# Performance work log

Measured on AMD Instinct MI355X. Metric: run time of the kernel, lower is better.

## Reference

```python
import math
import jax, jax.numpy as jnp
import numpy as np

BH, S, DK = 64, 1024, 64   # batch*heads, seq_len, head dim
FG, FL = 32, 32            # global / local enrichment feature dims
H, B = 16, 4               # mask layout [heads, batch, seq]


def setup_inputs() -> dict:
    key = jax.random.key(0)
    k1, k2, k3, k4, k5, k6 = jax.random.split(key, 6)
    return {
        "query": jax.random.normal(k1, (BH, S, DK), dtype=jnp.float32),
        "key": jax.random.normal(k2, (BH, S, DK), dtype=jnp.float32),
        "value": jax.random.normal(k3, (BH, S, DK), dtype=jnp.float32),
        "local_f": jax.random.normal(k4, (BH, S, FL), dtype=jnp.float32),
        "global_f": jax.random.normal(k5, (BH, S, FG), dtype=jnp.float32),
        "mask": jax.random.randint(k6, (H, B, S), 0, 2, dtype=jnp.int32),
    }


def reference(query, key, value, local_f, global_f, mask):
    dk = query.shape[-1]
    # enrich q/k with global then local features (matches torch concat order)
    pq = jnp.concatenate([query, global_f, local_f], axis=2)   # [BH, S, dk+fg+fl]
    pk = jnp.concatenate([key, global_f, local_f], axis=2)
    scores = jnp.einsum("bqd,bkd->bqk", pq, pk) / math.sqrt(dk)  # [BH, S, S]
    # mask [H, B, S] -> [H*B, S] -> broadcast over query positions
    m = mask.reshape(-1, mask.shape[-1])[:, None, :]            # [H*B, 1, S]
    scores = jnp.where(m == 1, jnp.float32(-1e9), scores)
    attn = jax.nn.softmax(scores, axis=-1)
    return jnp.einsum("bqk,bkd->bqd", attn, value)              # [BH, S, dk]
```

## Files before the change

kernel.cpp:

```cpp
#include <hip/hip_runtime.h>
#include <hip/hip_bf16.h>


#define BHn 64
#define Sn  1024
#define NT  16
#define KSTR 152
#define VSTR 72
#define KTILE (64*KSTR*2)
#define VTILE (64*VSTR*2)
#define BUFSZ (KTILE+VTILE)
#define OSTR 68
#define WAIT_VM0 0x0F70

typedef __attribute__((ext_vector_type(8)))  __bf16 bf16x8;
typedef __attribute__((ext_vector_type(16))) float  f32x16;
typedef __attribute__((ext_vector_type(4)))  unsigned int u32x4;

__device__ __forceinline__ unsigned f2bf1(float a){
    union { float f; unsigned u; } c; c.f = a;
    return (c.u + 0x7fffu + ((c.u >> 16) & 1u)) >> 16;
}
__device__ __forceinline__ unsigned f2bf2(float a, float b){
    return f2bf1(a) | (f2bf1(b) << 16);
}
__device__ __forceinline__ unsigned pkbf(float a, float b){
    return __builtin_amdgcn_perm(__builtin_bit_cast(unsigned, b),
                                 __builtin_bit_cast(unsigned, a), 0x07060302u);
}
__device__ __forceinline__ void gld_lds16(const void* g, void* l){
    __builtin_amdgcn_global_load_lds(
        (const __attribute__((address_space(1))) unsigned int*)g,
        (__attribute__((address_space(3))) unsigned int*)l, 16, 0, 0);
}

__global__ __launch_bounds__(256)
void attn_prep(const float* __restrict__ K, const float* __restrict__ V,
               const float* __restrict__ LF, const float* __restrict__ GF,
               const int* __restrict__ M,
               unsigned short* __restrict__ Kp, unsigned short* __restrict__ Vp)
{
    __shared__ __align__(16) unsigned char plds[BUFSZ];
    unsigned short* kl = (unsigned short*)plds;
    unsigned int*   vl = (unsigned int*)(plds + KTILE);

    const int tid = threadIdx.x;
    const int bh = blockIdx.x >> 4, ti = blockIdx.x & 15, kb = ti*64;

    #pragma unroll
    for (int i=0;i<2;i++){
        int idx = tid + 256*i, row = idx>>3, c = idx&7;
        const float* s = K + ((size_t)bh*Sn + kb + row)*64 + c*8;
        float4 f0 = *(const float4*)s, f1 = *(const float4*)(s+4);
        u32x4 w; w[0]=f2bf2(f0.x,f0.y); w[1]=f2bf2(f0.z,f0.w);
        w[2]=f2bf2(f1.x,f1.y); w[3]=f2bf2(f1.z,f1.w);
        *(u32x4*)(kl + row*KSTR + c*8) = w;
    }
    {
        int row = tid>>2, c = tid&3;
        const float* s = GF + ((size_t)bh*Sn + kb + row)*32 + c*8;
        float4 f0 = *(const float4*)s, f1 = *(const float4*)(s+4);
        u32x4 w; w[0]=f2bf2(f0.x,f0.y); w[1]=f2bf2(f0.z,f0.w);
        w[2]=f2bf2(f1.x,f1.y); w[3]=f2bf2(f1.z,f1.w);
        *(u32x4*)(kl + row*KSTR + 64 + c*8) = w;
    }
    {
        int row = tid>>2, c = tid&3;
        const float* s = LF + ((size_t)bh*Sn + kb + row)*32 + c*8;
        float4 f0 = *(const float4*)s, f1 = *(const float4*)(s+4);
        u32x4 w; w[0]=f2bf2(f0.x,f0.y); w[1]=f2bf2(f0.z,f0.w);
        w[2]=f2bf2(f1.x,f1.y); w[3]=f2bf2(f1.z,f1.w);
        *(u32x4*)(kl + row*KSTR + 96 + c*8) = w;
    }
    if (tid < 64){
        int mv = M[(size_t)bh*Sn + kb + tid];
        u32x4 w; w[0] = (mv == 1) ? 0x0000ceacu : 0u;
        w[1]=0u; w[2]=0u; w[3]=0u;
        *(u32x4*)(kl + tid*KSTR + 128) = w;
        u32x4 z; z[0]=0u; z[1]=0u; z[2]=0u; z[3]=0u;
        *(u32x4*)(kl + tid*KSTR + 136) = z;
        *(u32x4*)(kl + tid*KSTR + 144) = z;
    }
    {
        int d = tid & 63, g = tid >> 6;
        const float* vb = V + ((size_t)bh*Sn + kb + 16*g)*64 + d;
        const int pm[16] = {0,1,2,3, 8,9,10,11, 4,5,6,7, 12,13,14,15};
        unsigned w[8];
        #pragma unroll
        for (int m=0;m<8;m++)
            w[m] = f2bf2(vb[(size_t)pm[2*m]*64], vb[(size_t)pm[2*m+1]*64]);
        u32x4 a, b;
        a[0]=w[0]; a[1]=w[1]; a[2]=w[2]; a[3]=w[3];
        b[0]=w[4]; b[1]=w[5]; b[2]=w[6]; b[3]=w[7];
        *(u32x4*)(vl + d*36 + g*8)     = a;
        *(u32x4*)(vl + d*36 + g*8 + 4) = b;
        u32x4 z; z[0]=0u; z[1]=0u; z[2]=0u; z[3]=0u;
        *(u32x4*)(vl + d*36 + 32) = z;
    }
    __syncthreads();

    unsigned char* dK = (unsigned char*)Kp + (size_t)(bh*NT + ti)*KTILE;
    unsigned char* dV = (unsigned char*)Vp + (size_t)(bh*NT + ti)*VTILE;
    #pragma unroll
    for (int i=0;i<4;i++){
        int off = tid*16 + i*4096;
        *(u32x4*)(dK + off) = *(const u32x4*)(plds + off);
    }
    {
        int off = tid*16 + 4*4096;
        if (off < KTILE) *(u32x4*)(dK + off) = *(const u32x4*)(plds + off);
    }
    #pragma unroll
    for (int i=0;i<2;i++){
        int off = tid*16 + i*4096;
        *(u32x4*)(dV + off) = *(const u32x4*)(plds + KTILE + off);
    }
    {
        int off = tid*16 + 2*4096;
        if (off < VTILE) *(u32x4*)(dV + off) = *(const u32x4*)(plds + KTILE + off);
    }
}

__global__ __launch_bounds__(512, 4)
void attn_main(const float* __restrict__ Q, const unsigned short* __restrict__ Kp,
               const unsigned short* __restrict__ Vp,
               const float* __restrict__ GF, const float* __restrict__ LF,
               float* __restrict__ O)
{
    __shared__ __align__(16) unsigned char smem[2*BUFSZ];
    const int tid  = threadIdx.x;
    const int wave = tid >> 6, lane = tid & 63;
    const int l31  = lane & 31, h = lane >> 5;
    const int qh   = wave >> 1;
    const int kp   = wave & 1;
    const int bh = blockIdx.x & 63;
    const int qb = blockIdx.x >> 6;
    const float SCL = 0.18033688011112042f;

    const int qrow = qb*128 + qh*32 + l31;
    u32x4 qf[9];
    #pragma unroll
    for (int dc = 0; dc < 8; dc++){
        const int cb = dc*16 + 8*h;
        const float* src;
        if (cb < 64)      src = Q  + ((size_t)bh*Sn + qrow)*64 + cb;
        else if (cb < 96) src = GF + ((size_t)bh*Sn + qrow)*32 + (cb - 64);
        else              src = LF + ((size_t)bh*Sn + qrow)*32 + (cb - 96);
        float4 f0 = *(const float4*)src;
        float4 f1 = *(const float4*)(src + 4);
        qf[dc][0] = f2bf2(f0.x*SCL, f0.y*SCL);
        qf[dc][1] = f2bf2(f0.z*SCL, f0.w*SCL);
        qf[dc][2] = f2bf2(f1.x*SCL, f1.y*SCL);
        qf[dc][3] = f2bf2(f1.z*SCL, f1.w*SCL);
    }
    qf[8][0] = h ? 0u : 0x00003f80u;
    qf[8][1] = 0u; qf[8][2] = 0u; qf[8][3] = 0u;

    f32x16 oacc[2];
    #pragma unroll
    for (int dt=0; dt<2; dt++)
        #pragma unroll
        for (int r=0; r<16; r++) oacc[dt][r] = 0.f;
    float lrun = 0.f;

    const unsigned char* gKb = (const unsigned char*)Kp + (size_t)bh*NT*KTILE;
    const unsigned char* gVb = (const unsigned char*)Vp + (size_t)bh*NT*VTILE;

    #pragma unroll
    for (int i=0;i<4;i++){
        int c = wave + 8*i;
        if (c < 19)      gld_lds16(gKb + (size_t)c*1024 + lane*16, smem + c*1024);
        else if (c < 28) gld_lds16(gVb + (size_t)(c-19)*1024 + lane*16,
                                   smem + KTILE + (size_t)(c-19)*1024);
    }
    __builtin_amdgcn_s_waitcnt(WAIT_VM0);

    for (int t = 0; t < NT; t++){
        unsigned char* cur = smem + (size_t)(t&1)*BUFSZ;
        unsigned char* nxt = smem + (size_t)((t+1)&1)*BUFSZ;
        __syncthreads();
        if (t+1 < NT){
            const unsigned char* gK = gKb + (size_t)(t+1)*KTILE;
            const unsigned char* gV = gVb + (size_t)(t+1)*VTILE;
            #pragma unroll
            for (int i=0;i<4;i++){
                int c = wave + 8*i;
                if (c < 19)      gld_lds16(gK + (size_t)c*1024 + lane*16, nxt + c*1024);
                else if (c < 28) gld_lds16(gV + (size_t)(c-19)*1024 + lane*16,
                                           nxt + KTILE + (size_t)(c-19)*1024);
            }
        }
        unsigned short* kt_s = (unsigned short*)cur;
        unsigned short* vt_s = (unsigned short*)(cur + KTILE);

        f32x16 acc;
        #pragma unroll
        for (int r=0;r<16;r++) acc[r] = 0.f;
        #pragma unroll
        for (int dc=0; dc<9; dc++){
            u32x4 ar = *(const u32x4*)(kt_s + (kp*32 + l31)*KSTR + dc*16 + 8*h);
            acc = __builtin_amdgcn_mfma_f32_32x32x16_bf16(
                    __builtin_bit_cast(bf16x8, ar),
                    __builtin_bit_cast(bf16x8, qf[dc]), acc, 0, 0, 0);
        }

        float rs = 0.f;
        #pragma unroll
        for (int r=0;r<16;r++){
            float p = __builtin_amdgcn_exp2f(acc[r]);
            acc[r] = p; rs += p;
        }
        lrun += rs;

        unsigned pk[8];
        #pragma unroll
        for (int i=0;i<8;i++) pk[i] = pkbf(acc[2*i], acc[2*i+1]);
        u32x4 b0, b1;
        b0[0]=pk[0]; b0[1]=pk[1]; b0[2]=pk[2]; b0[3]=pk[3];
        b1[0]=pk[4]; b1[1]=pk[5]; b1[2]=pk[6]; b1[3]=pk[7];

        #pragma unroll
        for (int dt=0;dt<2;dt++){
            u32x4 va0 = *(const u32x4*)(vt_s + (dt*32 + l31)*VSTR + kp*32 + 8*h);
            u32x4 va1 = *(const u32x4*)(vt_s + (dt*32 + l31)*VSTR + kp*32 + 16 + 8*h);
            oacc[dt] = __builtin_amdgcn_mfma_f32_32x32x16_bf16(
                    __builtin_bit_cast(bf16x8, va0),
                    __builtin_bit_cast(bf16x8, b0), oacc[dt], 0, 0, 0);
            oacc[dt] = __builtin_amdgcn_mfma_f32_32x32x16_bf16(
                    __builtin_bit_cast(bf16x8, va1),
                    __builtin_bit_cast(bf16x8, b1), oacc[dt], 0, 0, 0);
        }

        __builtin_amdgcn_s_waitcnt(WAIT_VM0);
    }

    __syncthreads();
    float lw = lrun + __shfl_xor(lrun, 32, 64);
    float* s1 = (float*)smem;
    float* s2 = (float*)(smem + 128*OSTR*4);
    if (kp == 1){
        #pragma unroll
        for (int dt=0;dt<2;dt++)
            #pragma unroll
            for (int rg=0;rg<4;rg++){
                float4 w;
                w.x = oacc[dt][rg*4+0]; w.y = oacc[dt][rg*4+1];
                w.z = oacc[dt][rg*4+2]; w.w = oacc[dt][rg*4+3];
                *(float4*)(s1 + (qh*32 + l31)*OSTR + dt*32 + rg*8 + 4*h) = w;
            }
        if (h == 0) s2[qh*32 + l31] = lw;
    }
    __syncthreads();
    if (kp == 0){
        float inv = 1.0f / (lw + s2[qh*32 + l31]);
        #pragma unroll
        for (int dt=0;dt<2;dt++)
            #pragma unroll
            for (int rg=0;rg<4;rg++){
                float* p = s1 + (qh*32 + l31)*OSTR + dt*32 + rg*8 + 4*h;
                float4 w = *(float4*)p;
                w.x = (w.x + oacc[dt][rg*4+0])*inv;
                w.y = (w.y + oacc[dt][rg*4+1])*inv;
                w.z = (w.z + oacc[dt][rg*4+2])*inv;
                w.w = (w.w + oacc[dt][rg*4+3])*inv;
                *(float4*)p = w;
            }
    }
    __syncthreads();
    #pragma unroll
    for (int i=0;i<4;i++){
        int idx = tid + 512*i, r = idx>>4, c = idx&15;
        *(float4*)(O + ((size_t)bh*Sn + qb*128 + r)*64 + c*4) =
            *(const float4*)(s1 + r*OSTR + c*4);
    }
}

extern "C" void kernel_launch(void* const* d_in, const int* in_sizes, int n_in,
                              void* d_out, int out_size, void* d_ws, size_t ws_size,
                              hipStream_t stream) {
    const float* Q  = (const float*)d_in[0];
    const float* K  = (const float*)d_in[1];
    const float* V  = (const float*)d_in[2];
    const float* LF = (const float*)d_in[3];
    const float* GF = (const float*)d_in[4];
    const int*   M  = (const int*)d_in[5];
    float* O = (float*)d_out;

    unsigned short* Kp = (unsigned short*)d_ws;
    unsigned short* Vp = Kp + (size_t)BHn*NT*64*KSTR;

    attn_prep<<<dim3(BHn*NT), dim3(256), 0, stream>>>(K, V, LF, GF, M, Kp, Vp);
    attn_main<<<dim3(BHn*(Sn/128)), dim3(512), 0, stream>>>(Q, Kp, Vp, GF, LF, O);
}
```

Before: 140.7 us.

## Halve block to 4 waves, each computing two 32-row query subtiles

The main attention kernel now launches 256 threads (4 waves) per block instead of 512. Each wave handles two 32-row query subtiles and reuses every K and V fragment it reads from shared memory for two MFMAs, which halves LDS read traffic per FLOP. Each wave now issues 7 global-to-LDS loads per tile instead of up to 4, and the MFMA phases are wrapped in s_setprio. The cost is roughly double the accumulator and Q-fragment registers per wave and half as many waves per block to hide latency.

After: 144.3 us. 1.03x slower.

```diff
diff --git a/kernel.cpp b/kernel.cpp
--- a/kernel.cpp
+++ b/kernel.cpp
@@ -121,7 +121,7 @@
     }
 }
 
-__global__ __launch_bounds__(512, 4)
+__global__ __launch_bounds__(256, 2)
 void attn_main(const float* __restrict__ Q, const unsigned short* __restrict__ Kp,
                const unsigned short* __restrict__ Vp,
                const float* __restrict__ GF, const float* __restrict__ LF,
@@ -131,47 +131,53 @@
     const int tid  = threadIdx.x;
     const int wave = tid >> 6, lane = tid & 63;
     const int l31  = lane & 31, h = lane >> 5;
-    const int qh   = wave >> 1;
+    const int qp   = wave >> 1;
     const int kp   = wave & 1;
     const int bh = blockIdx.x & 63;
     const int qb = blockIdx.x >> 6;
     const float SCL = 0.18033688011112042f;
 
-    const int qrow = qb*128 + qh*32 + l31;
-    u32x4 qf[9];
-    #pragma unroll
-    for (int dc = 0; dc < 8; dc++){
-        const int cb = dc*16 + 8*h;
-        const float* src;
-        if (cb < 64)      src = Q  + ((size_t)bh*Sn + qrow)*64 + cb;
-        else if (cb < 96) src = GF + ((size_t)bh*Sn + qrow)*32 + (cb - 64);
-        else              src = LF + ((size_t)bh*Sn + qrow)*32 + (cb - 96);
-        float4 f0 = *(const float4*)src;
-        float4 f1 = *(const float4*)(src + 4);
-        qf[dc][0] = f2bf2(f0.x*SCL, f0.y*SCL);
-        qf[dc][1] = f2bf2(f0.z*SCL, f0.w*SCL);
-        qf[dc][2] = f2bf2(f1.x*SCL, f1.y*SCL);
-        qf[dc][3] = f2bf2(f1.z*SCL, f1.w*SCL);
-    }
-    qf[8][0] = h ? 0u : 0x00003f80u;
-    qf[8][1] = 0u; qf[8][2] = 0u; qf[8][3] = 0u;
-
-    f32x16 oacc[2];
-    #pragma unroll
-    for (int dt=0; dt<2; dt++)
-        #pragma unroll
-        for (int r=0; r<16; r++) oacc[dt][r] = 0.f;
-    float lrun = 0.f;
+    u32x4 qf[2][8];
+    #pragma unroll
+    for (int sub = 0; sub < 2; sub++){
+        const int qrow = qb*128 + qp*64 + sub*32 + l31;
+        #pragma unroll
+        for (int dc = 0; dc < 8; dc++){
+            const int cb = dc*16 + 8*h;
+            const float* src;
+            if (cb < 64)      src = Q  + ((size_t)bh*Sn + qrow)*64 + cb;
+            else if (cb < 96) src = GF + ((size_t)bh*Sn + qrow)*32 + (cb - 64);
+            else              src = LF + ((size_t)bh*Sn + qrow)*32 + (cb - 96);
+            float4 f0 = *(const float4*)src;
+            float4 f1 = *(const float4*)(src + 4);
+            qf[sub][dc][0] = f2bf2(f0.x*SCL, f0.y*SCL);
+            qf[sub][dc][1] = f2bf2(f0.z*SCL, f0.w*SCL);
+            qf[sub][dc][2] = f2bf2(f1.x*SCL, f1.y*SCL);
+            qf[sub][dc][3] = f2bf2(f1.z*SCL, f1.w*SCL);
+        }
+    }
+    u32x4 qfb;
+    qfb[0] = h ? 0u : 0x00003f80u;
+    qfb[1] = 0u; qfb[2] = 0u; qfb[3] = 0u;
+
+    f32x16 oacc[2][2];
+    #pragma unroll
+    for (int sub=0; sub<2; sub++)
+        #pragma unroll
+        for (int dt=0; dt<2; dt++)
+            #pragma unroll
+            for (int r=0; r<16; r++) oacc[sub][dt][r] = 0.f;
+    float lrun0 = 0.f, lrun1 = 0.f;
 
     const unsigned char* gKb = (const unsigned char*)Kp + (size_t)bh*NT*KTILE;
     const unsigned char* gVb = (const unsigned char*)Vp + (size_t)bh*NT*VTILE;
 
     #pragma unroll
-    for (int i=0;i<4;i++){
-        int c = wave + 8*i;
-        if (c < 19)      gld_lds16(gKb + (size_t)c*1024 + lane*16, smem + c*1024);
-        else if (c < 28) gld_lds16(gVb + (size_t)(c-19)*1024 + lane*16,
-                                   smem + KTILE + (size_t)(c-19)*1024);
+    for (int i=0;i<7;i++){
+        int c = wave + 4*i;
+        if (c < 19) gld_lds16(gKb + (size_t)c*1024 + lane*16, smem + c*1024);
+        else        gld_lds16(gVb + (size_t)(c-19)*1024 + lane*16,
+                              smem + KTILE + (size_t)(c-19)*1024);
     }
     __builtin_amdgcn_s_waitcnt(WAIT_VM0);
 
@@ -183,93 +189,133 @@
             const unsigned char* gK = gKb + (size_t)(t+1)*KTILE;
             const unsigned char* gV = gVb + (size_t)(t+1)*VTILE;
             #pragma unroll
-            for (int i=0;i<4;i++){
-                int c = wave + 8*i;
-                if (c < 19)      gld_lds16(gK + (size_t)c*1024 + lane*16, nxt + c*1024);
-                else if (c < 28) gld_lds16(gV + (size_t)(c-19)*1024 + lane*16,
-                                           nxt + KTILE + (size_t)(c-19)*1024);
+            for (int i=0;i<7;i++){
+                int c = wave + 4*i;
+                if (c < 19) gld_lds16(gK + (size_t)c*1024 + lane*16, nxt + c*1024);
+                else        gld_lds16(gV + (size_t)(c-19)*1024 + lane*16,
+                                      nxt + KTILE + (size_t)(c-19)*1024);
             }
         }
         unsigned short* kt_s = (unsigned short*)cur;
         unsigned short* vt_s = (unsigned short*)(cur + KTILE);
 
-        f32x16 acc;
-        #pragma unroll
-        for (int r=0;r<16;r++) acc[r] = 0.f;
-        #pragma unroll
-        for (int dc=0; dc<9; dc++){
+        f32x16 acc0, acc1;
+        #pragma unroll
+        for (int r=0;r<16;r++){ acc0[r] = 0.f; acc1[r] = 0.f; }
+        __builtin_amdgcn_s_setprio(1);
+        #pragma unroll
+        for (int dc=0; dc<8; dc++){
             u32x4 ar = *(const u32x4*)(kt_s + (kp*32 + l31)*KSTR + dc*16 + 8*h);
-            acc = __builtin_amdgcn_mfma_f32_32x32x16_bf16(
+            acc0 = __builtin_amdgcn_mfma_f32_32x32x16_bf16(
                     __builtin_bit_cast(bf16x8, ar),
-                    __builtin_bit_cast(bf16x8, qf[dc]), acc, 0, 0, 0);
-        }
-
-        float rs = 0.f;
+                    __builtin_bit_cast(bf16x8, qf[0][dc]), acc0, 0, 0, 0);
+            acc1 = __builtin_amdgcn_mfma_f32_32x32x16_bf16(
+                    __builtin_bit_cast(bf16x8, ar),
+                    __builtin_bit_cast(bf16x8, qf[1][dc]), acc1, 0, 0, 0);
+        }
+        {
+            u32x4 ab = *(const u32x4*)(kt_s + (kp*32 + l31)*KSTR + 128 + 8*h);
+            acc0 = __builtin_amdgcn_mfma_f32_32x32x16_bf16(
+                    __builtin_bit_cast(bf16x8, ab),
+                    __builtin_bit_cast(bf16x8, qfb), acc0, 0, 0, 0);
+            acc1 = __builtin_amdgcn_mfma_f32_32x32x16_bf16(
+                    __builtin_bit_cast(bf16x8, ab),
+                    __builtin_bit_cast(bf16x8, qfb), acc1, 0, 0, 0);
+        }
+        __builtin_amdgcn_s_setprio(0);
+
+        float rs0 = 0.f, rs1 = 0.f;
         #pragma unroll
         for (int r=0;r<16;r++){
-            float p = __builtin_amdgcn_exp2f(acc[r]);
-            acc[r] = p; rs += p;
-        }
-        lrun += rs;
-
-        unsigned pk[8];
-        #pragma unroll
-        for (int i=0;i<8;i++) pk[i] = pkbf(acc[2*i], acc[2*i+1]);
-        u32x4 b0, b1;
-        b0[0]=pk[0]; b0[1]=pk[1]; b0[2]=pk[2]; b0[3]=pk[3];
-        b1[0]=pk[4]; b1[1]=pk[5]; b1[2]=pk[6]; b1[3]=pk[7];
-
+            float p0 = __builtin_amdgcn_exp2f(acc0[r]);
+            float p1 = __builtin_amdgcn_exp2f(acc1[r]);
+            acc0[r] = p0; rs0 += p0;
+            acc1[r] = p1; rs1 += p1;
+        }
+        lrun0 += rs0; lrun1 += rs1;
+
+        unsigned pk0[8], pk1[8];
+        #pragma unroll
+        for (int i=0;i<8;i++){
+            pk0[i] = pkbf(acc0[2*i], acc0[2*i+1]);
+            pk1[i] = pkbf(acc1[2*i], acc1[2*i+1]);
+        }
+        u32x4 b00, b01, b10, b11;
+        b00[0]=pk0[0]; b00[1]=pk0[1]; b00[2]=pk0[2]; b00[3]=pk0[3];
+        b01[0]=pk0[4]; b01[1]=pk0[5]; b01[2]=pk0[6]; b01[3]=pk0[7];
+        b10[0]=pk1[0]; b10[1]=pk1[1]; b10[2]=pk1[2]; b10[3]=pk1[3];
+        b11[0]=pk1[4]; b11[1]=pk1[5]; b11[2]=pk1[6]; b11[3]=pk1[7];
+
+        __builtin_amdgcn_s_setprio(1);
         #pragma unroll
         for (int dt=0;dt<2;dt++){
             u32x4 va0 = *(const u32x4*)(vt_s + (dt*32 + l31)*VSTR + kp*32 + 8*h);
             u32x4 va1 = *(const u32x4*)(vt_s + (dt*32 + l31)*VSTR + kp*32 + 16 + 8*h);
-            oacc[dt] = __builtin_amdgcn_mfma_f32_32x32x16_bf16(
+            oacc[0][dt] = __builtin_amdgcn_mfma_f32_32x32x16_bf16(
                     __builtin_bit_cast(bf16x8, va0),
-                    __builtin_bit_cast(bf16x8, b0), oacc[dt], 0, 0, 0);
-            oacc[dt] = __builtin_amdgcn_mfma_f32_32x32x16_bf16(
+                    __builtin_bit_cast(bf16x8, b00), oacc[0][dt], 0, 0, 0);
+            oacc[0][dt] = __builtin_amdgcn_mfma_f32_32x32x16_bf16(
                     __builtin_bit_cast(bf16x8, va1),
-                    __builtin_bit_cast(bf16x8, b1), oacc[dt], 0, 0, 0);
-        }
+                    __builtin_bit_cast(bf16x8, b01), oacc[0][dt], 0, 0, 0);
+            oacc[1][dt] = __builtin_amdgcn_mfma_f32_32x32x16_bf16(
+                    __builtin_bit_cast(bf16x8, va0),
+                    __builtin_bit_cast(bf16x8, b10), oacc[1][dt], 0, 0, 0);
+            oacc[1][dt] = __builtin_amdgcn_mfma_f32_32x32x16_bf16(
+                    __builtin_bit_cast(bf16x8, va1),
+                    __builtin_bit_cast(bf16x8, b11), oacc[1][dt], 0, 0, 0);
+        }
+        __builtin_amdgcn_s_setprio(0);
 
         __builtin_amdgcn_s_waitcnt(WAIT_VM0);
     }
 
     __syncthreads();
-    float lw = lrun + __shfl_xor(lrun, 32, 64);
+    float lw0 = lrun0 + __shfl_xor(lrun0, 32, 64);
+    float lw1 = lrun1 + __shfl_xor(lrun1, 32, 64);
     float* s1 = (float*)smem;
     float* s2 = (float*)(smem + 128*OSTR*4);
     if (kp == 1){
         #pragma unroll
-        for (int dt=0;dt<2;dt++)
+        for (int sub=0;sub<2;sub++)
             #pragma unroll
-            for (int rg=0;rg<4;rg++){
-                float4 w;
-                w.x = oacc[dt][rg*4+0]; w.y = oacc[dt][rg*4+1];
-                w.z = oacc[dt][rg*4+2]; w.w = oacc[dt][rg*4+3];
-                *(float4*)(s1 + (qh*32 + l31)*OSTR + dt*32 + rg*8 + 4*h) = w;
-            }
-        if (h == 0) s2[qh*32 + l31] = lw;
+            for (int dt=0;dt<2;dt++)
+                #pragma unroll
+                for (int rg=0;rg<4;rg++){
+                    float4 w;
+                    w.x = oacc[sub][dt][rg*4+0]; w.y = oacc[sub][dt][rg*4+1];
+                    w.z = oacc[sub][dt][rg*4+2]; w.w = oacc[sub][dt][rg*4+3];
+                    *(float4*)(s1 + (qp*64 + sub*32 + l31)*OSTR + dt*32 + rg*8 + 4*h) = w;
+                }
+        if (h == 0){
+            s2[qp*64 + l31]      = lw0;
+            s2[qp*64 + 32 + l31] = lw1;
+        }
     }
     __syncthreads();
     if (kp == 0){
-        float inv = 1.0f / (lw + s2[qh*32 + l31]);
-        #pragma unroll
-        for (int dt=0;dt<2;dt++)
+        float inv0 = 1.0f / (lw0 + s2[qp*64 + l31]);
+        float inv1 = 1.0f / (lw1 + s2[qp*64 + 32 + l31]);
+        #pragma unroll
+        for (int sub=0;sub<2;sub++){
+            float inv = sub ? inv1 : inv0;
             #pragma unroll
-            for (int rg=0;rg<4;rg++){
-                float* p = s1 + (qh*32 + l31)*OSTR + dt*32 + rg*8 + 4*h;
-                float4 w = *(float4*)p;
-                w.x = (w.x + oacc[dt][rg*4+0])*inv;
-                w.y = (w.y + oacc[dt][rg*4+1])*inv;
-                w.z = (w.z + oacc[dt][rg*4+2])*inv;
-                w.w = (w.w + oacc[dt][rg*4+3])*inv;
-                *(float4*)p = w;
-            }
+            for (int dt=0;dt<2;dt++)
+                #pragma unroll
+                for (int rg=0;rg<4;rg++){
+                    float* p = s1 + (qp*64 + sub*32 + l31)*OSTR + dt*32 + rg*8 + 4*h;
+                    float4 w = *(float4*)p;
+                    w.x = (w.x + oacc[sub][dt][rg*4+0])*inv;
+                    w.y = (w.y + oacc[sub][dt][rg*4+1])*inv;
+                    w.z = (w.z + oacc[sub][dt][rg*4+2])*inv;
+                    w.w = (w.w + oacc[sub][dt][rg*4+3])*inv;
+                    *(float4*)p = w;
+                }
+        }
     }
     __syncthreads();
     #pragma unroll
-    for (int i=0;i<4;i++){
-        int idx = tid + 512*i, r = idx>>4, c = idx&15;
+    for (int i=0;i<8;i++){
+        int idx = tid + 256*i, r = idx>>4, c = idx&15;
         *(float4*)(O + ((size_t)bh*Sn + qb*128 + r)*64 + c*4) =
             *(const float4*)(s1 + r*OSTR + c*4);
     }
@@ -290,5 +336,5 @@
     unsigned short* Vp = Kp + (size_t)BHn*NT*64*KSTR;
 
     attn_prep<<<dim3(BHn*NT), dim3(256), 0, stream>>>(K, V, LF, GF, M, Kp, Vp);
-    attn_main<<<dim3(BHn*(Sn/128)), dim3(512), 0, stream>>>(Q, Kp, Vp, GF, LF, O);
-}
+    attn_main<<<dim3(BHn*(Sn/128)), dim3(256), 0, stream>>>(Q, Kp, Vp, GF, LF, O);
+}
```

## Pre-swizzle K/V tiles into MFMA fragment layout and load directly from global

Applied to the files above, without the earlier changes.

The prep kernel now writes K (with features and mask column) and V into a single packed buffer laid out exactly as the MFMA operand fragments each lane needs. The main kernel then reads operands straight from global/L2 with coalesced 16-byte loads instead of staging double-buffered tiles through LDS. This removes the per-tile barriers and LDS traffic and shrinks shared memory use. It also adds s_setprio around the MFMA bursts and a tree-reduced row sum. The risk is that global-load latency is no longer hidden by an explicit prefetch, and each K/V tile is now read by every wave separately through cache.

Measured after the change: 146.5 us. 4.1% more time.

```diff
diff --git a/kernel.cpp b/kernel.cpp
--- a/kernel.cpp
+++ b/kernel.cpp
@@ -5,13 +5,9 @@
 #define BHn 64
 #define Sn  1024
 #define NT  16
-#define KSTR 152
-#define VSTR 72
-#define KTILE (64*KSTR*2)
-#define VTILE (64*VSTR*2)
-#define BUFSZ (KTILE+VTILE)
+#define TILESZ 26624
+#define KIMG   18432
 #define OSTR 68
-#define WAIT_VM0 0x0F70
 
 typedef __attribute__((ext_vector_type(8)))  __bf16 bf16x8;
 typedef __attribute__((ext_vector_type(16))) float  f32x16;
@@ -28,21 +24,13 @@
     return __builtin_amdgcn_perm(__builtin_bit_cast(unsigned, b),
                                  __builtin_bit_cast(unsigned, a), 0x07060302u);
 }
-__device__ __forceinline__ void gld_lds16(const void* g, void* l){
-    __builtin_amdgcn_global_load_lds(
-        (const __attribute__((address_space(1))) unsigned int*)g,
-        (__attribute__((address_space(3))) unsigned int*)l, 16, 0, 0);
-}
 
 __global__ __launch_bounds__(256)
 void attn_prep(const float* __restrict__ K, const float* __restrict__ V,
                const float* __restrict__ LF, const float* __restrict__ GF,
-               const int* __restrict__ M,
-               unsigned short* __restrict__ Kp, unsigned short* __restrict__ Vp)
+               const int* __restrict__ M, unsigned short* __restrict__ P)
 {
-    __shared__ __align__(16) unsigned char plds[BUFSZ];
-    unsigned short* kl = (unsigned short*)plds;
-    unsigned int*   vl = (unsigned int*)(plds + KTILE);
+    __shared__ __align__(16) unsigned char plds[TILESZ];
 
     const int tid = threadIdx.x;
     const int bh = blockIdx.x >> 4, ti = blockIdx.x & 15, kb = ti*64;
@@ -54,32 +42,35 @@
         float4 f0 = *(const float4*)s, f1 = *(const float4*)(s+4);
         u32x4 w; w[0]=f2bf2(f0.x,f0.y); w[1]=f2bf2(f0.z,f0.w);
         w[2]=f2bf2(f1.x,f1.y); w[3]=f2bf2(f1.z,f1.w);
-        *(u32x4*)(kl + row*KSTR + c*8) = w;
-    }
-    {
-        int row = tid>>2, c = tid&3;
-        const float* s = GF + ((size_t)bh*Sn + kb + row)*32 + c*8;
+        int kp = row>>5, l31 = row&31, dc = c>>1, h = c&1;
+        *(u32x4*)(plds + ((kp*9+dc)*2+h)*512 + l31*16) = w;
+    }
+    {
+        int row = tid>>2, c2 = tid&3;
+        const float* s = GF + ((size_t)bh*Sn + kb + row)*32 + c2*8;
         float4 f0 = *(const float4*)s, f1 = *(const float4*)(s+4);
         u32x4 w; w[0]=f2bf2(f0.x,f0.y); w[1]=f2bf2(f0.z,f0.w);
         w[2]=f2bf2(f1.x,f1.y); w[3]=f2bf2(f1.z,f1.w);
-        *(u32x4*)(kl + row*KSTR + 64 + c*8) = w;
-    }
-    {
-        int row = tid>>2, c = tid&3;
-        const float* s = LF + ((size_t)bh*Sn + kb + row)*32 + c*8;
+        int kp = row>>5, l31 = row&31, dc = 4+(c2>>1), h = c2&1;
+        *(u32x4*)(plds + ((kp*9+dc)*2+h)*512 + l31*16) = w;
+    }
+    {
+        int row = tid>>2, c2 = tid&3;
+        const float* s = LF + ((size_t)bh*Sn + kb + row)*32 + c2*8;
         float4 f0 = *(const float4*)s, f1 = *(const float4*)(s+4);
         u32x4 w; w[0]=f2bf2(f0.x,f0.y); w[1]=f2bf2(f0.z,f0.w);
         w[2]=f2bf2(f1.x,f1.y); w[3]=f2bf2(f1.z,f1.w);
-        *(u32x4*)(kl + row*KSTR + 96 + c*8) = w;
+        int kp = row>>5, l31 = row&31, dc = 6+(c2>>1), h = c2&1;
+        *(u32x4*)(plds + ((kp*9+dc)*2+h)*512 + l31*16) = w;
     }
     if (tid < 64){
         int mv = M[(size_t)bh*Sn + kb + tid];
+        int kp = tid>>5, l31 = tid&31;
         u32x4 w; w[0] = (mv == 1) ? 0x0000ceacu : 0u;
         w[1]=0u; w[2]=0u; w[3]=0u;
-        *(u32x4*)(kl + tid*KSTR + 128) = w;
+        *(u32x4*)(plds + ((kp*9+8)*2+0)*512 + l31*16) = w;
         u32x4 z; z[0]=0u; z[1]=0u; z[2]=0u; z[3]=0u;
-        *(u32x4*)(kl + tid*KSTR + 136) = z;
-        *(u32x4*)(kl + tid*KSTR + 144) = z;
+        *(u32x4*)(plds + ((kp*9+8)*2+1)*512 + l31*16) = z;
     }
     {
         int d = tid & 63, g = tid >> 6;
@@ -92,42 +83,31 @@
         u32x4 a, b;
         a[0]=w[0]; a[1]=w[1]; a[2]=w[2]; a[3]=w[3];
         b[0]=w[4]; b[1]=w[5]; b[2]=w[6]; b[3]=w[7];
-        *(u32x4*)(vl + d*36 + g*8)     = a;
-        *(u32x4*)(vl + d*36 + g*8 + 4) = b;
-        u32x4 z; z[0]=0u; z[1]=0u; z[2]=0u; z[3]=0u;
-        *(u32x4*)(vl + d*36 + 32) = z;
-    }
-    __syncthreads();
-
-    unsigned char* dK = (unsigned char*)Kp + (size_t)(bh*NT + ti)*KTILE;
-    unsigned char* dV = (unsigned char*)Vp + (size_t)(bh*NT + ti)*VTILE;
-    #pragma unroll
-    for (int i=0;i<4;i++){
+        int kp = g>>1, j = g&1, dt = d>>5, l31 = d&31;
+        unsigned char* vs = plds + KIMG + (((kp*2+dt)*2+j)*2)*512 + l31*16;
+        *(u32x4*)(vs)       = a;
+        *(u32x4*)(vs + 512) = b;
+    }
+    __syncthreads();
+
+    unsigned char* dP = (unsigned char*)P + (size_t)(bh*NT + ti)*TILESZ;
+    #pragma unroll
+    for (int i=0;i<6;i++){
         int off = tid*16 + i*4096;
-        *(u32x4*)(dK + off) = *(const u32x4*)(plds + off);
-    }
-    {
-        int off = tid*16 + 4*4096;
-        if (off < KTILE) *(u32x4*)(dK + off) = *(const u32x4*)(plds + off);
-    }
-    #pragma unroll
-    for (int i=0;i<2;i++){
-        int off = tid*16 + i*4096;
-        *(u32x4*)(dV + off) = *(const u32x4*)(plds + KTILE + off);
-    }
-    {
-        int off = tid*16 + 2*4096;
-        if (off < VTILE) *(u32x4*)(dV + off) = *(const u32x4*)(plds + KTILE + off);
+        *(u32x4*)(dP + off) = *(const u32x4*)(plds + off);
+    }
+    {
+        int off = tid*16 + 6*4096;
+        if (off < TILESZ) *(u32x4*)(dP + off) = *(const u32x4*)(plds + off);
     }
 }
 
 __global__ __launch_bounds__(512, 4)
-void attn_main(const float* __restrict__ Q, const unsigned short* __restrict__ Kp,
-               const unsigned short* __restrict__ Vp,
+void attn_main(const float* __restrict__ Q, const unsigned short* __restrict__ P,
                const float* __restrict__ GF, const float* __restrict__ LF,
                float* __restrict__ O)
 {
-    __shared__ __align__(16) unsigned char smem[2*BUFSZ];
+    __shared__ __align__(16) unsigned char smem[128*OSTR*4 + 512];
     const int tid  = threadIdx.x;
     const int wave = tid >> 6, lane = tid & 63;
     const int l31  = lane & 31, h = lane >> 5;
@@ -163,75 +143,64 @@
         for (int r=0; r<16; r++) oacc[dt][r] = 0.f;
     float lrun = 0.f;
 
-    const unsigned char* gKb = (const unsigned char*)Kp + (size_t)bh*NT*KTILE;
-    const unsigned char* gVb = (const unsigned char*)Vp + (size_t)bh*NT*VTILE;
-
-    #pragma unroll
-    for (int i=0;i<4;i++){
-        int c = wave + 8*i;
-        if (c < 19)      gld_lds16(gKb + (size_t)c*1024 + lane*16, smem + c*1024);
-        else if (c < 28) gld_lds16(gVb + (size_t)(c-19)*1024 + lane*16,
-                                   smem + KTILE + (size_t)(c-19)*1024);
-    }
-    __builtin_amdgcn_s_waitcnt(WAIT_VM0);
+    const unsigned char* kptr = (const unsigned char*)P
+        + (size_t)bh*NT*TILESZ + kp*9216 + lane*16;
+    const unsigned char* vptr = (const unsigned char*)P
+        + (size_t)bh*NT*TILESZ + KIMG + kp*4096 + lane*16;
 
     for (int t = 0; t < NT; t++){
-        unsigned char* cur = smem + (size_t)(t&1)*BUFSZ;
-        unsigned char* nxt = smem + (size_t)((t+1)&1)*BUFSZ;
-        __syncthreads();
-        if (t+1 < NT){
-            const unsigned char* gK = gKb + (size_t)(t+1)*KTILE;
-            const unsigned char* gV = gVb + (size_t)(t+1)*VTILE;
-            #pragma unroll
-            for (int i=0;i<4;i++){
-                int c = wave + 8*i;
-                if (c < 19)      gld_lds16(gK + (size_t)c*1024 + lane*16, nxt + c*1024);
-                else if (c < 28) gld_lds16(gV + (size_t)(c-19)*1024 + lane*16,
-                                           nxt + KTILE + (size_t)(c-19)*1024);
-            }
-        }
-        unsigned short* kt_s = (unsigned short*)cur;
-        unsigned short* vt_s = (unsigned short*)(cur + KTILE);
+        const unsigned char* kt = kptr + (size_t)t*TILESZ;
+        const unsigned char* vt = vptr + (size_t)t*TILESZ;
 
         f32x16 acc;
         #pragma unroll
         for (int r=0;r<16;r++) acc[r] = 0.f;
+        __builtin_amdgcn_s_setprio(1);
         #pragma unroll
         for (int dc=0; dc<9; dc++){
-            u32x4 ar = *(const u32x4*)(kt_s + (kp*32 + l31)*KSTR + dc*16 + 8*h);
+            u32x4 ar = *(const u32x4*)(kt + dc*1024);
             acc = __builtin_amdgcn_mfma_f32_32x32x16_bf16(
                     __builtin_bit_cast(bf16x8, ar),
                     __builtin_bit_cast(bf16x8, qf[dc]), acc, 0, 0, 0);
         }
-
-        float rs = 0.f;
-        #pragma unroll
-        for (int r=0;r<16;r++){
-            float p = __builtin_amdgcn_exp2f(acc[r]);
-            acc[r] = p; rs += p;
-        }
-        lrun += rs;
+        __builtin_amdgcn_s_setprio(0);
+
+        u32x4 va00 = *(const u32x4*)(vt);
+        u32x4 va01 = *(const u32x4*)(vt + 1024);
+        u32x4 va10 = *(const u32x4*)(vt + 2048);
+        u32x4 va11 = *(const u32x4*)(vt + 3072);
+
+        float p[16];
+        #pragma unroll
+        for (int r=0;r<16;r++) p[r] = __builtin_amdgcn_exp2f(acc[r]);
+        float s4[8];
+        #pragma unroll
+        for (int r=0;r<8;r++) s4[r] = p[2*r] + p[2*r+1];
+        #pragma unroll
+        for (int r=0;r<4;r++) s4[r] = s4[2*r] + s4[2*r+1];
+        lrun += (s4[0]+s4[1]) + (s4[2]+s4[3]);
 
         unsigned pk[8];
         #pragma unroll
-        for (int i=0;i<8;i++) pk[i] = pkbf(acc[2*i], acc[2*i+1]);
+        for (int i=0;i<8;i++) pk[i] = pkbf(p[2*i], p[2*i+1]);
         u32x4 b0, b1;
         b0[0]=pk[0]; b0[1]=pk[1]; b0[2]=pk[2]; b0[3]=pk[3];
         b1[0]=pk[4]; b1[1]=pk[5]; b1[2]=pk[6]; b1[3]=pk[7];
 
-        #pragma unroll
-        for (int dt=0;dt<2;dt++){
-            u32x4 va0 = *(const u32x4*)(vt_s + (dt*32 + l31)*VSTR + kp*32 + 8*h);
-            u32x4 va1 = *(const u32x4*)(vt_s + (dt*32 + l31)*VSTR + kp*32 + 16 + 8*h);
-            oacc[dt] = __builtin_amdgcn_mfma_f32_32x32x16_bf16(
-                    __builtin_bit_cast(bf16x8, va0),
-                    __builtin_bit_cast(bf16x8, b0), oacc[dt], 0, 0, 0);
-            oacc[dt] = __builtin_amdgcn_mfma_f32_32x32x16_bf16(
-                    __builtin_bit_cast(bf16x8, va1),
-                    __builtin_bit_cast(bf16x8, b1), oacc[dt], 0, 0, 0);
-        }
-
-        __builtin_amdgcn_s_waitcnt(WAIT_VM0);
+        __builtin_amdgcn_s_setprio(1);
+        oacc[0] = __builtin_amdgcn_mfma_f32_32x32x16_bf16(
+                __builtin_bit_cast(bf16x8, va00),
+                __builtin_bit_cast(bf16x8, b0), oacc[0], 0, 0, 0);
+        oacc[0] = __builtin_amdgcn_mfma_f32_32x32x16_bf16(
+                __builtin_bit_cast(bf16x8, va01),
+                __builtin_bit_cast(bf16x8, b1), oacc[0], 0, 0, 0);
+        oacc[1] = __builtin_amdgcn_mfma_f32_32x32x16_bf16(
+                __builtin_bit_cast(bf16x8, va10),
+                __builtin_bit_cast(bf16x8, b0), oacc[1], 0, 0, 0);
+        oacc[1] = __builtin_amdgcn_mfma_f32_32x32x16_bf16(
+                __builtin_bit_cast(bf16x8, va11),
+                __builtin_bit_cast(bf16x8, b1), oacc[1], 0, 0, 0);
+        __builtin_amdgcn_s_setprio(0);
     }
 
     __syncthreads();
@@ -286,9 +255,8 @@
     const int*   M  = (const int*)d_in[5];
     float* O = (float*)d_out;
 
-    unsigned short* Kp = (unsigned short*)d_ws;
-    unsigned short* Vp = Kp + (size_t)BHn*NT*64*KSTR;
-
-    attn_prep<<<dim3(BHn*NT), dim3(256), 0, stream>>>(K, V, LF, GF, M, Kp, Vp);
-    attn_main<<<dim3(BHn*(Sn/128)), dim3(512), 0, stream>>>(Q, Kp, Vp, GF, LF, O);
-}
+    unsigned short* P = (unsigned short*)d_ws;
+
+    attn_prep<<<dim3(BHn*NT), dim3(256), 0, stream>>>(K, V, LF, GF, M, P);
+    attn_main<<<dim3(BHn*(Sn/128)), dim3(512), 0, stream>>>(Q, P, GF, LF, O);
+}
```
